# Optimization experiments

Hardware: AMD Instinct MI355X
Metric: run time of the kernel (lower is better)

The kernel has to match this reference:

```python
import jax, jax.numpy as jnp
import numpy as np

N, C, G, M, E = 100000, 8, 8, 32, 1600000
EPS = 1e-8


def setup_inputs() -> dict:
    key = jax.random.key(0)
    k1, k2, k3, k4, k5 = jax.random.split(key, 5)
    x = jax.random.randint(k1, (N,), 0, M)
    prev_h = jax.random.uniform(k2, (N, C, G), dtype=jnp.float32)
    edge_index = jax.random.randint(k3, (2, E), 0, N)
    Q_neigh = jax.random.normal(k4, (C, C, G), dtype=jnp.float32) * 1.25
    B = jax.random.normal(k5, (C, M, G), dtype=jnp.float32) * 1.25
    return {"x": x, "prev_h": prev_h, "edge_index": edge_index,
            "Q_neigh": Q_neigh, "B": B}


def reference(x, prev_h, edge_index, Q_neigh, B):
    n = prev_h.shape[0]
    # softmax reparameterization (vectorized over n_gen)
    Qs = jax.nn.softmax(Q_neigh, axis=0)          # [C, C, G], columns sum to 1 over dim 0
    Bs = jax.nn.softmax(B, axis=1)                # [C, M, G], rows sum to 1 over M

    dst, src = edge_index[0], edge_index[1]
    neigh = prev_h[src]                            # [E, C, G] gather
    summed = jax.ops.segment_sum(neigh, dst, num_segments=n)            # [N, C, G]
    counts = jax.ops.segment_sum(jnp.ones((src.shape[0],), prev_h.dtype), dst,
                                 num_segments=n)                        # [N]
    aggr = summed / jnp.maximum(counts, 1.0)[:, None, None]             # scatter-mean, 0 for isolated nodes

    B_nodes = jnp.transpose(Bs[:, x], (1, 0, 2))[:, :, None, :]         # [N, C, 1, G]
    unnorm = B_nodes * (Qs[None, :, :, :] * aggr[:, None, :, :]) + EPS  # [N, C, C, G]

    denom = unnorm.sum(axis=(1, 2), keepdims=True)                      # [N, 1, 1, G]
    posterior_il = unnorm / denom
    posterior_i = posterior_il.sum(axis=2)                              # [N, C, G]
    likelihood = jnp.log(jnp.squeeze(denom, (1, 2)))                    # [N, G]
    return likelihood, posterior_i
```

## Files before the change

kernel.cpp:

```cpp
#include <hip/hip_runtime.h>

#define C_    8
#define G_    8
#define CG    64
#define CAP   48
#define CELL  56
#define BSPAN 256
#define SBLK  256
#define CVT   160
#define BG    512
#define Z1    1720
#define Z2    1280
#define ZTOT  4096
#define EPSF  1e-8f

__device__ __forceinline__ unsigned short bf16rne(float v) {
    unsigned u = __float_as_uint(v);
    return (unsigned short)((u + 0x7FFFu + ((u >> 16) & 1u)) >> 16);
}
__device__ __forceinline__ float bf16tof(unsigned short h) {
    return __uint_as_float((unsigned)h << 16);
}

__device__ __forceinline__ void zsum_block(int zgid, const float* __restrict__ Bmat,
                                           float* __restrict__ Z, int M) {
    if (zgid >= ZTOT) return;
    __shared__ float zpart[4][8];
    int c = zgid & 7, bx = zgid >> 3;
    const float4* B4 = (const float4*)(Bmat + (size_t)c * M * G_);
    const int total4 = M * 2;
    int tid = bx * 256 + threadIdx.x;
    const int zstride = (ZTOT / 8) * 256;
    float a0 = 0.f, a1 = 0.f, a2 = 0.f, a3 = 0.f;
    for (int f = tid; f < total4; f += zstride) {
        float4 v = B4[f];
        a0 += __expf(v.x); a1 += __expf(v.y); a2 += __expf(v.z); a3 += __expf(v.w);
    }
    #pragma unroll
    for (int m = 2; m <= 32; m <<= 1) {
        a0 += __shfl_xor(a0, m, 64);
        a1 += __shfl_xor(a1, m, 64);
        a2 += __shfl_xor(a2, m, 64);
        a3 += __shfl_xor(a3, m, 64);
    }
    int lane = threadIdx.x & 63, w = threadIdx.x >> 6;
    if (lane < 2) {
        int g0 = lane * 4;
        zpart[w][g0 + 0] = a0; zpart[w][g0 + 1] = a1;
        zpart[w][g0 + 2] = a2; zpart[w][g0 + 3] = a3;
    }
    __syncthreads();
    if (threadIdx.x < 8) {
        float s = zpart[0][threadIdx.x] + zpart[1][threadIdx.x]
                + zpart[2][threadIdx.x] + zpart[3][threadIdx.x];
        atomicAdd(&Z[c * G_ + threadIdx.x], s);
    }
}

__global__ void k_d1(const int* __restrict__ ei, int E, int npart,
                     int* __restrict__ counts, int* __restrict__ staging,
                     const float* __restrict__ prev_h, unsigned short* __restrict__ ph16,
                     int N, const float* __restrict__ Qn, float* __restrict__ Qs,
                     const int* __restrict__ x, unsigned short* __restrict__ blog16,
                     const float* __restrict__ Bmat, float* __restrict__ Z, int M) {
    int b = blockIdx.x;
    if (b < SBLK) {
        __shared__ int cur[512];
        for (int p = threadIdx.x; p < npart; p += 256) cur[p] = 0;
        __syncthreads();
        int chunk = (E + SBLK - 1) / SBLK;
        int lo = b * chunk, hi = min(E, lo + chunk);
        for (int e = lo + threadIdx.x; e < hi; e += 256) {
            int dst = ei[e], src = ei[E + e];
            int p = dst >> 8;
            int c = atomicAdd(&cur[p], 1);
            if (c < CELL) staging[(p * SBLK + b) * CELL + c] = ((dst & 255) << 23) | src;
        }
        __syncthreads();
        for (int p = threadIdx.x; p < npart; p += 256)
            counts[p * SBLK + b] = cur[p];
    } else if (b < SBLK + CVT) {
        int gid = (b - SBLK) * 256 + threadIdx.x;
        int total8 = N * 8;
        const int cstride = CVT * 256;
        for (int f = gid; f < total8; f += cstride) {
            const float4* s = (const float4*)(prev_h + (size_t)f * 8);
            float4 v0 = s[0], v1 = s[1];
            float vv[8] = {v0.x, v0.y, v0.z, v0.w, v1.x, v1.y, v1.z, v1.w};
            unsigned r[4];
            #pragma unroll
            for (int k = 0; k < 4; ++k)
                r[k] = (unsigned)bf16rne(vv[2 * k]) | ((unsigned)bf16rne(vv[2 * k + 1]) << 16);
            *(uint4*)(ph16 + (size_t)f * 8) = make_uint4(r[0], r[1], r[2], r[3]);
        }
    } else if (b == SBLK + CVT) {
        __shared__ float e[512];
        __shared__ float cs[64];
        int t = threadIdx.x;
        e[t] = __expf(Qn[t]); e[t + 256] = __expf(Qn[t + 256]);
        __syncthreads();
        if (t < 64) {
            float s = 0.f;
            #pragma unroll
            for (int i2 = 0; i2 < 8; ++i2) s += e[i2 * 64 + t];
            cs[t] = s;
        }
        __syncthreads();
        Qs[t] = e[t] / cs[t & 63];
        Qs[t + 256] = e[t + 256] / cs[t & 63];
    } else if (b < SBLK + CVT + 1 + BG) {
        int gidx = b - (SBLK + CVT + 1);
        int lane = threadIdx.x & 63, w = threadIdx.x >> 6;
        int i = lane >> 3, g = lane & 7;
        const int step = BG * 4 * 4;
        for (int n0 = (gidx * 4 + w) * 4; n0 < N; n0 += step) {
            int xs[4];
            #pragma unroll
            for (int k = 0; k < 4; ++k) xs[k] = (n0 + k < N) ? x[n0 + k] : 0;
            #pragma unroll
            for (int k = 0; k < 4; ++k)
                if (n0 + k < N)
                    blog16[(size_t)(n0 + k) * CG + lane] =
                        bf16rne(Bmat[((size_t)i * M + xs[k]) * G_ + g]);
        }
    } else {
        zsum_block(b - (SBLK + CVT + 1 + BG), Bmat, Z, M);
    }
}

__global__ void k_d2(const int* __restrict__ counts, const int* __restrict__ staging,
                     int* __restrict__ cnt, int* __restrict__ csr, int N, int npart,
                     const float* __restrict__ Bmat, float* __restrict__ Z, int M) {
    int b = blockIdx.x;
    if (b >= npart) { zsum_block(Z1 + (b - npart), Bmat, Z, M); return; }
    __shared__ int cl[BSPAN];
    __shared__ int csl[BSPAN * CAP];
    int t = threadIdx.x;
    cl[t] = 0;
    __syncthreads();
    int cnum = min(counts[b * SBLK + t], CELL);
    int cbase = (b * SBLK + t) * CELL;
    for (int j = 0; j < cnum; ++j) {
        int v = staging[cbase + j];
        int local = (unsigned)v >> 23;
        int src = v & 0x7FFFFF;
        int pos = atomicAdd(&cl[local], 1);
        if (pos < CAP) csl[local * CAP + pos] = src;
    }
    __syncthreads();
    int n = b * BSPAN + t;
    if (n < N) cnt[n] = cl[t];
    for (int idx = t; idx < BSPAN * CAP; idx += 256)
        csr[(size_t)b * (BSPAN * CAP) + idx] = csl[idx];
}

__global__ void k_ti(const unsigned short* __restrict__ ph16, const int* __restrict__ cnt,
                     const int* __restrict__ csr, const float* __restrict__ Qs,
                     unsigned short* __restrict__ ti16,
                     const float* __restrict__ Bmat, float* __restrict__ Z,
                     int M, int N, int nAggr) {
    int b = blockIdx.x;
    if (b >= nAggr) { zsum_block(Z1 + Z2 + (b - nAggr), Bmat, Z, M); return; }
    int lane = threadIdx.x & 63, w = threadIdx.x >> 6;
    int i = lane >> 3, g = lane & 7;
    int base = b * 16 + w * 4;
    if (base >= N) return;
    int nk[4]; bool valid[4]; int deg[4], dl[4], nb[4];
    #pragma unroll
    for (int k = 0; k < 4; ++k) {
        int n = base + k;
        valid[k] = (n < N);
        nk[k] = valid[k] ? n : (N - 1);
    }
    #pragma unroll
    for (int k = 0; k < 4; ++k) {
        deg[k] = valid[k] ? cnt[nk[k]] : 0;
        dl[k]  = min(deg[k], CAP);
        nb[k]  = dl[k] >> 2;
    }
    float q[8];
    #pragma unroll
    for (int l = 0; l < 8; ++l) q[l] = Qs[i * 64 + l * 8 + g];
    float acc[4] = {0.f, 0.f, 0.f, 0.f};
    int nbmax = max(max(nb[0], nb[1]), max(nb[2], nb[3]));
    for (int q2 = 0; q2 < nbmax; ++q2) {
        #pragma unroll
        for (int k = 0; k < 4; ++k) {
            if (q2 < nb[k]) {
                int4 s4 = ((const int4*)(csr + (size_t)nk[k] * CAP))[q2];
                acc[k] += bf16tof(ph16[(s4.x << 6) | lane]);
                acc[k] += bf16tof(ph16[(s4.y << 6) | lane]);
                acc[k] += bf16tof(ph16[(s4.z << 6) | lane]);
                acc[k] += bf16tof(ph16[(s4.w << 6) | lane]);
            }
        }
    }
    #pragma unroll
    for (int k = 0; k < 4; ++k) {
        const int* crow = csr + (size_t)nk[k] * CAP;
        for (int e2 = nb[k] * 4; e2 < dl[k]; ++e2)
            acc[k] += bf16tof(ph16[(crow[e2] << 6) | lane]);
    }
    #pragma unroll
    for (int k = 0; k < 4; ++k) {
        float aggr = (deg[k] > 0) ? acc[k] / (float)deg[k] : 0.f;
        float ti = 0.f;
        #pragma unroll
        for (int l = 0; l < 8; ++l) ti += q[l] * __shfl(aggr, l * 8 + g, 64);
        if (valid[k]) ti16[(size_t)nk[k] * CG + lane] = bf16rne(ti);
    }
}

__global__ void k_epi(const unsigned short* __restrict__ ti16,
                      const unsigned short* __restrict__ blog16,
                      const float* __restrict__ Z, float* __restrict__ out, int N) {
    int w = threadIdx.x >> 6, lane = threadIdx.x & 63;
    int i = lane >> 3, g = lane & 7;
    int base = (blockIdx.x * 4 + w) * 4;
    if (base >= N) return;
    float invZ = 1.f / Z[lane];
    #pragma unroll
    for (int k = 0; k < 4; ++k) {
        int n = base + k;
        if (n >= N) break;
        float ti = bf16tof(ti16[(size_t)n * CG + lane]);
        float bl = bf16tof(blog16[(size_t)n * CG + lane]);
        float u = __expf(bl) * invZ * ti;
        float s = u;
        #pragma unroll
        for (int m = 8; m <= 32; m <<= 1) s += __shfl_xor(s, m, 64);
        float denom = s + 64.f * EPSF;
        if (i == 0) out[n * G_ + g] = logf(denom);
        out[(size_t)N * G_ + (size_t)n * CG + lane] = (u + 8.f * EPSF) / denom;
    }
}

extern "C" void kernel_launch(void* const* d_in, const int* in_sizes, int n_in,
                              void* d_out, int out_size, void* d_ws, size_t ws_size,
                              hipStream_t stream) {
    const int*   x      = (const int*)d_in[0];
    const float* prev_h = (const float*)d_in[1];
    const int*   ei     = (const int*)d_in[2];
    const float* Qn     = (const float*)d_in[3];
    const float* Bm     = (const float*)d_in[4];
    float* out = (float*)d_out;

    int N = in_sizes[0];
    int E = in_sizes[2] / 2;
    int M = in_sizes[4] / CG;
    int npart = (N + BSPAN - 1) / BSPAN;
    int nAggr = (N + 15) / 16;

    float* Z      = (float*)d_ws;
    float* Qs     = Z + 64;
    int*   counts = (int*)d_ws + 576;
    int*   cnt    = counts + npart * SBLK;
    int*   stag   = cnt + N;
    int*   csr    = stag + (size_t)npart * SBLK * CELL;
    unsigned short* ph16   = (unsigned short*)(csr + (size_t)npart * BSPAN * CAP);
    unsigned short* blog16 = ph16 + (size_t)N * CG;
    unsigned short* ti16   = blog16 + (size_t)N * CG;

    hipMemsetAsync(d_ws, 0, 64 * sizeof(float), stream);

    k_d1<<<SBLK + CVT + 1 + BG + Z1, 256, 0, stream>>>(
        ei, E, npart, counts, stag, prev_h, ph16, N, Qn, Qs, x, blog16, Bm, Z, M);
    k_d2<<<npart + Z2, 256, 0, stream>>>(counts, stag, cnt, csr, N, npart, Bm, Z, M);
    k_ti<<<nAggr + (ZTOT - Z1 - Z2), 256, 0, stream>>>(ph16, cnt, csr, Qs, ti16,
                                                       Bm, Z, M, N, nAggr);
    k_epi<<<(N + 15) / 16, 256, 0, stream>>>(ti16, blog16, Z, out, N);
}
```

Baseline: 145.3 us.

## Fuse epilogue into aggregation kernel and move Z-sum blocks earlier

Merges the epilogue kernel into the aggregation kernel, so the per-node transform result is used directly instead of being written to and re-read from a bf16 scratch buffer. The Z normalisation blocks that previously ran alongside aggregation are now split entirely between the first two kernels, so Z is complete before the fused kernel reads it. This removes one launch and one round trip of N*64 bf16 values through memory. The cost is more Z-sum work in the two earlier kernels, which may lengthen them.

After: 141.0 us (median of 2 runs). 1.03x faster.

```diff
diff --git a/kernel.cpp b/kernel.cpp
--- a/kernel.cpp
+++ b/kernel.cpp
@@ -9,8 +9,8 @@
 #define SBLK  256
 #define CVT   160
 #define BG    512
-#define Z1    1720
-#define Z2    1280
+#define Z1    2048
+#define Z2    2048
 #define ZTOT  4096
 #define EPSF  1e-8f
 
@@ -156,15 +156,13 @@
 
 __global__ void k_ti(const unsigned short* __restrict__ ph16, const int* __restrict__ cnt,
                      const int* __restrict__ csr, const float* __restrict__ Qs,
-                     unsigned short* __restrict__ ti16,
-                     const float* __restrict__ Bmat, float* __restrict__ Z,
-                     int M, int N, int nAggr) {
-    int b = blockIdx.x;
-    if (b >= nAggr) { zsum_block(Z1 + Z2 + (b - nAggr), Bmat, Z, M); return; }
+                     const unsigned short* __restrict__ blog16,
+                     const float* __restrict__ Z, float* __restrict__ out, int N) {
     int lane = threadIdx.x & 63, w = threadIdx.x >> 6;
     int i = lane >> 3, g = lane & 7;
-    int base = b * 16 + w * 4;
+    int base = blockIdx.x * 16 + w * 4;
     if (base >= N) return;
+    float invZ = 1.f / Z[lane];
     int nk[4]; bool valid[4]; int deg[4], dl[4], nb[4];
     #pragma unroll
     for (int k = 0; k < 4; ++k) {
@@ -207,31 +205,16 @@
         float ti = 0.f;
         #pragma unroll
         for (int l = 0; l < 8; ++l) ti += q[l] * __shfl(aggr, l * 8 + g, 64);
-        if (valid[k]) ti16[(size_t)nk[k] * CG + lane] = bf16rne(ti);
-    }
-}
-
-__global__ void k_epi(const unsigned short* __restrict__ ti16,
-                      const unsigned short* __restrict__ blog16,
-                      const float* __restrict__ Z, float* __restrict__ out, int N) {
-    int w = threadIdx.x >> 6, lane = threadIdx.x & 63;
-    int i = lane >> 3, g = lane & 7;
-    int base = (blockIdx.x * 4 + w) * 4;
-    if (base >= N) return;
-    float invZ = 1.f / Z[lane];
-    #pragma unroll
-    for (int k = 0; k < 4; ++k) {
-        int n = base + k;
-        if (n >= N) break;
-        float ti = bf16tof(ti16[(size_t)n * CG + lane]);
-        float bl = bf16tof(blog16[(size_t)n * CG + lane]);
+        float bl = bf16tof(blog16[(size_t)nk[k] * CG + lane]);
         float u = __expf(bl) * invZ * ti;
         float s = u;
         #pragma unroll
         for (int m = 8; m <= 32; m <<= 1) s += __shfl_xor(s, m, 64);
         float denom = s + 64.f * EPSF;
-        if (i == 0) out[n * G_ + g] = logf(denom);
-        out[(size_t)N * G_ + (size_t)n * CG + lane] = (u + 8.f * EPSF) / denom;
+        if (valid[k]) {
+            if (i == 0) out[nk[k] * G_ + g] = logf(denom);
+            out[(size_t)N * G_ + (size_t)nk[k] * CG + lane] = (u + 8.f * EPSF) / denom;
+        }
     }
 }
 
@@ -259,14 +242,11 @@
     int*   csr    = stag + (size_t)npart * SBLK * CELL;
     unsigned short* ph16   = (unsigned short*)(csr + (size_t)npart * BSPAN * CAP);
     unsigned short* blog16 = ph16 + (size_t)N * CG;
-    unsigned short* ti16   = blog16 + (size_t)N * CG;
 
     hipMemsetAsync(d_ws, 0, 64 * sizeof(float), stream);
 
     k_d1<<<SBLK + CVT + 1 + BG + Z1, 256, 0, stream>>>(
         ei, E, npart, counts, stag, prev_h, ph16, N, Qn, Qs, x, blog16, Bm, Z, M);
     k_d2<<<npart + Z2, 256, 0, stream>>>(counts, stag, cnt, csr, N, npart, Bm, Z, M);
-    k_ti<<<nAggr + (ZTOT - Z1 - Z2), 256, 0, stream>>>(ph16, cnt, csr, Qs, ti16,
-                                                       Bm, Z, M, N, nAggr);
-    k_epi<<<(N + 15) / 16, 256, 0, stream>>>(ti16, blog16, Z, out, N);
-}
+    k_ti<<<nAggr, 256, 0, stream>>>(ph16, cnt, csr, Qs, blog16, Z, out, N);
+}
```
